# Kernel optimization log

Hardware: AMD Instinct MI355X
Metric: run time of the kernel (lower is better)

The kernel has to match this reference:

```python
import jax, jax.numpy as jnp
import numpy as np
from functools import partial

B, C, IMG, P = 16, 1, 512, 16
GRID = IMG // P           # 32
N = GRID * GRID           # 1024
E = 768
DEPTH = 12
H = 12
HD = E // H               # 64
FF = 4 * E                # 3072
NUM_KEEP = N // 2         # mask_ratio = 0.5
LN_EPS = 1e-5


def sincos_2d_pos_embed(embed_dim, grid_size):
    half = embed_dim // 2
    def emb1d(dim, pos):
        hd = dim // 2
        freq = jnp.exp(-np.log(10000.0) * jnp.arange(hd, dtype=jnp.float32) / hd)
        ang = pos[:, None] * freq[None, :]
        return jnp.concatenate([jnp.sin(ang), jnp.cos(ang)], axis=1)
    gh, gw = jnp.meshgrid(jnp.arange(grid_size, dtype=jnp.float32),
                          jnp.arange(grid_size, dtype=jnp.float32), indexing='ij')
    return jnp.concatenate([emb1d(half, gh.reshape(-1)), emb1d(half, gw.reshape(-1))], axis=1)


def setup_inputs() -> dict:
    key = jax.random.key(0)
    ks = jax.random.split(key, 16)
    std = 0.02
    d = {
        'x': jax.random.normal(ks[0], (B, C, IMG, IMG), jnp.float32),
        'noise': jax.random.uniform(ks[1], (B, N), jnp.float32),
        'patch_w': jax.random.normal(ks[2], (E, C, P, P), jnp.float32) * std,
        'patch_b': jnp.zeros((E,), jnp.float32),
        'pe_norm_w': jnp.ones((E,), jnp.float32),
        'pe_norm_b': jnp.zeros((E,), jnp.float32),
        'pos_embed': sincos_2d_pos_embed(E, GRID)[None],  # [1, N, E]
        'ln1_w': jnp.ones((DEPTH, E), jnp.float32),
        'ln1_b': jnp.zeros((DEPTH, E), jnp.float32),
        'qkv_w': jax.random.normal(ks[3], (DEPTH, 3 * E, E), jnp.float32) * std,
        'qkv_b': jnp.zeros((DEPTH, 3 * E), jnp.float32),
        'proj_w': jax.random.normal(ks[4], (DEPTH, E, E), jnp.float32) * std,
        'proj_b': jnp.zeros((DEPTH, E), jnp.float32),
        'ln2_w': jnp.ones((DEPTH, E), jnp.float32),
        'ln2_b': jnp.zeros((DEPTH, E), jnp.float32),
        'fc1_w': jax.random.normal(ks[5], (DEPTH, FF, E), jnp.float32) * std,
        'fc1_b': jnp.zeros((DEPTH, FF), jnp.float32),
        'fc2_w': jax.random.normal(ks[6], (DEPTH, E, FF), jnp.float32) * std,
        'fc2_b': jnp.zeros((DEPTH, E), jnp.float32),
        'norm_w': jnp.ones((E,), jnp.float32),
        'norm_b': jnp.zeros((E,), jnp.float32),
    }
    return d


def layernorm(x, w, b):
    m = jnp.mean(x, axis=-1, keepdims=True)
    v = jnp.mean(jnp.square(x - m), axis=-1, keepdims=True)
    return (x - m) * jax.lax.rsqrt(v + LN_EPS) * w + b


def transformer_block(x, p):
    ln1_w, ln1_b, qkv_w, qkv_b, proj_w, proj_b, ln2_w, ln2_b, fc1_w, fc1_b, fc2_w, fc2_b = p
    b, n, _ = x.shape
    h = layernorm(x, ln1_w, ln1_b)
    qkv = (h @ qkv_w.T + qkv_b).reshape(b, n, 3, H, HD)
    q, k, v = qkv[:, :, 0], qkv[:, :, 1], qkv[:, :, 2]          # [b, n, H, HD]
    scale = HD ** -0.5
    attn = jnp.einsum('bqhd,bkhd->bhqk', q, k) * scale
    attn = jax.nn.softmax(attn, axis=-1)
    o = jnp.einsum('bhqk,bkhd->bqhd', attn, v).reshape(b, n, E)
    x = x + (o @ proj_w.T + proj_b)
    h = layernorm(x, ln2_w, ln2_b)
    h = jax.nn.gelu(h @ fc1_w.T + fc1_b, approximate=False)
    x = x + (h @ fc2_w.T + fc2_b)
    return x


def reference(x, noise, patch_w, patch_b, pe_norm_w, pe_norm_b, pos_embed,
              ln1_w, ln1_b, qkv_w, qkv_b, proj_w, proj_b,
              ln2_w, ln2_b, fc1_w, fc1_b, fc2_w, fc2_b, norm_w, norm_b):
    b = x.shape[0]
    # Patch embedding: stride-P conv == patch extraction + matmul
    patches = x.reshape(b, C, GRID, P, GRID, P).transpose(0, 2, 4, 1, 3, 5)
    patches = patches.reshape(b, N, C * P * P)
    t = patches @ patch_w.reshape(E, -1).T + patch_b            # [b, N, E]
    t = layernorm(t, pe_norm_w, pe_norm_b)
    t = t + pos_embed
    # Random masking (mask_ratio = 0.5)
    ids_shuffle = jnp.argsort(noise, axis=1)
    ids_restore = jnp.argsort(ids_shuffle, axis=1)
    ids_keep = ids_shuffle[:, :NUM_KEEP]
    x_vis = jnp.take_along_axis(t, ids_keep[:, :, None], axis=1)  # [b, NUM_KEEP, E]
    mask = jnp.ones((b, N), jnp.float32).at[:, :NUM_KEEP].set(0.0)
    mask = jnp.take_along_axis(mask, ids_restore, axis=1)
    # Transformer blocks (scan over stacked per-layer params)
    stacked = (ln1_w, ln1_b, qkv_w, qkv_b, proj_w, proj_b,
               ln2_w, ln2_b, fc1_w, fc1_b, fc2_w, fc2_b)
    def body(carry, p):
        return transformer_block(carry, p), None
    x_vis, _ = jax.lax.scan(body, x_vis, stacked)
    x_vis = layernorm(x_vis, norm_w, norm_b)
    return x_vis, mask, ids_restore
```

## Files before the change

kernel.cpp:

```cpp
#include <hip/hip_runtime.h>
#include <hip/hip_bf16.h>
#include <cstddef>
#include <cstdint>

typedef unsigned short u16;
typedef __attribute__((ext_vector_type(8))) short short8;
typedef __attribute__((ext_vector_type(4))) float f32x4;

constexpr int BB   = 16;
constexpr int E    = 768;
constexpr int DEPTH= 12;
constexpr int NH   = 12;
constexpr int FF   = 3072;
constexpr int NTOK = 1024;
constexpr int KEEP = 512;
constexpr float LN_EPS = 1e-5f;

__device__ __forceinline__ u16 f2b(float f) {
    __hip_bfloat16 h = __float2bfloat16(f);
    return *reinterpret_cast<u16*>(&h);
}

__global__ __launch_bounds__(256)
void patchify16(const float* __restrict__ x, u16* __restrict__ patches) {
    int i = blockIdx.x * 256 + threadIdx.x;
    int k = i & 255;
    int n = (i >> 8) & 1023;
    int b = i >> 18;
    int gi = n >> 5, gj = n & 31;
    int pi = k >> 4, pj = k & 15;
    patches[i] = f2b(x[((size_t)b << 18) + (size_t)((gi << 4) + pi) * 512 + (gj << 4) + pj]);
}

__global__ __launch_bounds__(256)
void convert4(const float* __restrict__ s0, int n0, const float* __restrict__ s1, int n1,
              const float* __restrict__ s2, int n2, const float* __restrict__ s3, int n3,
              u16* __restrict__ dst, int total) {
    int i4 = (blockIdx.x * 256 + threadIdx.x) * 4;
    if (i4 >= total) return;
    const float* s; int off;
    if (i4 < n0) { s = s0; off = i4; }
    else if (i4 < n0 + n1) { s = s1; off = i4 - n0; }
    else if (i4 < n0 + n1 + n2) { s = s2; off = i4 - n0 - n1; }
    else { s = s3; off = i4 - n0 - n1 - n2; }
    float4 v = *(const float4*)(s + off);
    u16 u0 = f2b(v.x), u1 = f2b(v.y), u2 = f2b(v.z), u3 = f2b(v.w);
    u16 tmp[4] = {u0, u1, u2, u3};
    *(uint2*)(dst + i4) = *(uint2*)tmp;
}

__device__ __forceinline__ float block_sum256(float v, float* sh) {
    #pragma unroll
    for (int m = 32; m; m >>= 1) v += __shfl_xor(v, m, 64);
    int w = threadIdx.x >> 6;
    __syncthreads();
    if ((threadIdx.x & 63) == 0) sh[w] = v;
    __syncthreads();
    return sh[0] + sh[1] + sh[2] + sh[3];
}

template<bool OUTBF, bool POS>
__global__ __launch_bounds__(256)
void ln_kernel(const float* __restrict__ in, void* __restrict__ outp,
               const float* __restrict__ w, const float* __restrict__ bias,
               const float* __restrict__ pos) {
    __shared__ float sh[4];
    int tok = blockIdx.x, t = threadIdx.x;
    const float* row = in + (size_t)tok * E;
    float v0 = row[t], v1 = row[t + 256], v2 = row[t + 512];
    float s = block_sum256(v0 + v1 + v2, sh);
    float mean = s * (1.0f / 768.0f);
    float d0 = v0 - mean, d1 = v1 - mean, d2 = v2 - mean;
    float s2 = block_sum256(d0*d0 + d1*d1 + d2*d2, sh);
    float rstd = rsqrtf(s2 * (1.0f / 768.0f) + LN_EPS);
    float r0 = d0 * rstd * w[t]       + bias[t];
    float r1 = d1 * rstd * w[t + 256] + bias[t + 256];
    float r2 = d2 * rstd * w[t + 512] + bias[t + 512];
    if (POS) {
        int n = tok & (NTOK - 1);
        const float* prow = pos + (size_t)n * E;
        r0 += prow[t]; r1 += prow[t + 256]; r2 += prow[t + 512];
    }
    if (OUTBF) {
        u16* orow = (u16*)outp + (size_t)tok * E;
        orow[t] = f2b(r0); orow[t + 256] = f2b(r1); orow[t + 512] = f2b(r2);
    } else {
        float* orow = (float*)outp + (size_t)tok * E;
        orow[t] = r0; orow[t + 256] = r1; orow[t + 512] = r2;
    }
}

__global__ __launch_bounds__(1024)
void sort_kernel(const float* __restrict__ noise, int* __restrict__ ids_keep,
                 float* __restrict__ mask_out, float* __restrict__ restore_out) {
    __shared__ float sv[1024];
    __shared__ int   si[1024];
    int b = blockIdx.x, t = threadIdx.x;
    sv[t] = noise[b * 1024 + t];
    si[t] = t;
    __syncthreads();
    for (int k = 2; k <= 1024; k <<= 1) {
        for (int j = k >> 1; j > 0; j >>= 1) {
            int p = t ^ j;
            if (p > t) {
                bool up = ((t & k) == 0);
                float a = sv[t], c = sv[p];
                int ia = si[t], ic = si[p];
                bool sw = up ? (a > c || (a == c && ia > ic))
                             : (a < c || (a == c && ia < ic));
                if (sw) { sv[t] = c; sv[p] = a; si[t] = ic; si[p] = ia; }
            }
            __syncthreads();
        }
    }
    int idx = si[t];
    if (t < KEEP) ids_keep[b * KEEP + t] = idx;
    restore_out[b * 1024 + idx] = (float)t;
    mask_out[b * 1024 + idx] = (t < KEEP) ? 0.0f : 1.0f;
}

__global__ __launch_bounds__(256)
void gather_kernel(const float* __restrict__ t, const int* __restrict__ keep,
                   float* __restrict__ X) {
    int tok = blockIdx.x;
    int b = tok >> 9;
    int src = keep[tok];
    const float* s = t + ((size_t)(b << 10) + src) * E;
    float* d = X + (size_t)tok * E;
    int tid = threadIdx.x;
    d[tid]       = s[tid];
    d[tid + 256] = s[tid + 256];
    d[tid + 512] = s[tid + 512];
}

template<bool GELU, bool RES, bool OUTBF>
__global__ __launch_bounds__(256)
void mfma_gemm(const u16* __restrict__ A, const u16* __restrict__ W,
               const float* __restrict__ bias, const float* __restrict__ R,
               void* __restrict__ Cout, int M, int N, int K) {
    __shared__ u16 As[128 * 32];
    __shared__ u16 Ws[128 * 32];
    int tid = threadIdx.x;
    int lane = tid & 63, w = tid >> 6;
    int m0 = blockIdx.y << 7, n0 = blockIdx.x << 7;
    int wr = (w >> 1) << 6;
    int wc = (w & 1) << 6;
    int r16 = lane & 15, kq = lane >> 4;

    f32x4 acc[4][4];
    #pragma unroll
    for (int i = 0; i < 4; ++i)
        #pragma unroll
        for (int j = 0; j < 4; ++j) acc[i][j] = (f32x4)0.0f;

    int seg = w * 2;
    const u16* gA = A + (size_t)(m0 + seg * 16 + (lane >> 2)) * K + (lane & 3) * 8;
    const u16* gW = W + (size_t)(n0 + seg * 16 + (lane >> 2)) * K + (lane & 3) * 8;
    u16* lA = As + seg * 512;
    u16* lW = Ws + seg * 512;
    const size_t rowK16 = (size_t)16 * K;

    for (int k0 = 0; k0 < K; k0 += 32) {
        __syncthreads();
        __builtin_amdgcn_global_load_lds((const __attribute__((address_space(1))) void*)(gA + k0),
                                         (__attribute__((address_space(3))) void*)(lA), 16, 0, 0);
        __builtin_amdgcn_global_load_lds((const __attribute__((address_space(1))) void*)(gA + k0 + rowK16),
                                         (__attribute__((address_space(3))) void*)(lA + 512), 16, 0, 0);
        __builtin_amdgcn_global_load_lds((const __attribute__((address_space(1))) void*)(gW + k0),
                                         (__attribute__((address_space(3))) void*)(lW), 16, 0, 0);
        __builtin_amdgcn_global_load_lds((const __attribute__((address_space(1))) void*)(gW + k0 + rowK16),
                                         (__attribute__((address_space(3))) void*)(lW + 512), 16, 0, 0);
        __syncthreads();
        short8 af[4], bf[4];
        #pragma unroll
        for (int t = 0; t < 4; ++t) af[t] = *(const short8*)(As + (wr + t * 16 + r16) * 32 + kq * 8);
        #pragma unroll
        for (int t = 0; t < 4; ++t) bf[t] = *(const short8*)(Ws + (wc + t * 16 + r16) * 32 + kq * 8);
        #pragma unroll
        for (int i = 0; i < 4; ++i)
            #pragma unroll
            for (int j = 0; j < 4; ++j)
                acc[i][j] = __builtin_amdgcn_mfma_f32_16x16x32_bf16(af[i], bf[j], acc[i][j], 0, 0, 0);
    }

    #pragma unroll
    for (int i = 0; i < 4; ++i) {
        int row = m0 + wr + i * 16 + kq * 4;
        #pragma unroll
        for (int j = 0; j < 4; ++j) {
            int col = n0 + wc + j * 16 + r16;
            float bcol = bias[col];
            #pragma unroll
            for (int rg = 0; rg < 4; ++rg) {
                size_t off = (size_t)(row + rg) * N + col;
                float v = acc[i][j][rg] + bcol;
                if (GELU) v = 0.5f * v * (1.0f + erff(v * 0.70710678118654752f));
                if (RES)  v += R[off];
                if (OUTBF) ((u16*)Cout)[off] = f2b(v);
                else       ((float*)Cout)[off] = v;
            }
        }
    }
}

__global__ __launch_bounds__(256)
void attn_mfma(const u16* __restrict__ qkv, u16* __restrict__ out) {
    __shared__ u16 Ks[64 * 80];
    __shared__ u16 Vt[64 * 80];
    __shared__ u16 Ps[64 * 80];
    int tid = threadIdx.x, lane = tid & 63, w = tid >> 6;
    int bh = blockIdx.y;
    int b = bh / NH, h = bh - b * NH;
    int q0 = blockIdx.x << 6;
    int r16 = lane & 15, kq = lane >> 4;
    const u16* base = qkv + (size_t)b * 512 * 2304 + h * 64;

    const u16* qrow = base + (size_t)(q0 + w * 16 + r16) * 2304 + kq * 8;
    short8 qa0 = *(const short8*)(qrow);
    short8 qa1 = *(const short8*)(qrow + 32);

    f32x4 o[4];
    #pragma unroll
    for (int dt = 0; dt < 4; ++dt) o[dt] = (f32x4)0.0f;
    float mrow[4], lrow[4];
    #pragma unroll
    for (int r = 0; r < 4; ++r) { mrow[r] = -1e30f; lrow[r] = 0.0f; }

    for (int kt = 0; kt < 8; ++kt) {
        int k0 = kt << 6;
        __syncthreads();
        #pragma unroll
        for (int i = 0; i < 2; ++i) {
            int v = tid + 256 * i;
            int kp = v >> 3, d8 = (v & 7) * 8;
            short8 kv = *(const short8*)(base + (size_t)(k0 + kp) * 2304 + 768 + d8);
            *(short8*)(Ks + kp * 80 + d8) = kv;
            short8 vv = *(const short8*)(base + (size_t)(k0 + kp) * 2304 + 1536 + d8);
            #pragma unroll
            for (int j = 0; j < 8; ++j) Vt[(d8 + j) * 80 + kp] = (u16)vv[j];
        }
        __syncthreads();
        f32x4 s[4];
        #pragma unroll
        for (int ct = 0; ct < 4; ++ct) {
            short8 kb0 = *(const short8*)(Ks + (ct * 16 + r16) * 80 + kq * 8);
            short8 kb1 = *(const short8*)(Ks + (ct * 16 + r16) * 80 + kq * 8 + 32);
            s[ct] = (f32x4)0.0f;
            s[ct] = __builtin_amdgcn_mfma_f32_16x16x32_bf16(qa0, kb0, s[ct], 0, 0, 0);
            s[ct] = __builtin_amdgcn_mfma_f32_16x16x32_bf16(qa1, kb1, s[ct], 0, 0, 0);
            s[ct] *= 0.125f;
        }
        float alpha[4];
        #pragma unroll
        for (int r = 0; r < 4; ++r) {
            float mx = fmaxf(fmaxf(s[0][r], s[1][r]), fmaxf(s[2][r], s[3][r]));
            #pragma unroll
            for (int msk = 1; msk < 16; msk <<= 1) mx = fmaxf(mx, __shfl_xor(mx, msk, 64));
            float mnew = fmaxf(mrow[r], mx);
            alpha[r] = expf(mrow[r] - mnew);
            mrow[r] = mnew;
            float ls = 0.0f;
            #pragma unroll
            for (int ct = 0; ct < 4; ++ct) {
                float p = expf(s[ct][r] - mnew);
                s[ct][r] = p; ls += p;
            }
            #pragma unroll
            for (int msk = 1; msk < 16; msk <<= 1) ls += __shfl_xor(ls, msk, 64);
            lrow[r] = lrow[r] * alpha[r] + ls;
        }
        #pragma unroll
        for (int ct = 0; ct < 4; ++ct)
            #pragma unroll
            for (int r = 0; r < 4; ++r)
                Ps[(w * 16 + kq * 4 + r) * 80 + ct * 16 + r16] = f2b(s[ct][r]);
        #pragma unroll
        for (int dt = 0; dt < 4; ++dt)
            #pragma unroll
            for (int r = 0; r < 4; ++r) o[dt][r] *= alpha[r];
        short8 pa0 = *(const short8*)(Ps + (w * 16 + r16) * 80 + kq * 8);
        short8 pa1 = *(const short8*)(Ps + (w * 16 + r16) * 80 + kq * 8 + 32);
        #pragma unroll
        for (int dt = 0; dt < 4; ++dt) {
            short8 vb0 = *(const short8*)(Vt + (dt * 16 + r16) * 80 + kq * 8);
            short8 vb1 = *(const short8*)(Vt + (dt * 16 + r16) * 80 + kq * 8 + 32);
            o[dt] = __builtin_amdgcn_mfma_f32_16x16x32_bf16(pa0, vb0, o[dt], 0, 0, 0);
            o[dt] = __builtin_amdgcn_mfma_f32_16x16x32_bf16(pa1, vb1, o[dt], 0, 0, 0);
        }
    }
    #pragma unroll
    for (int dt = 0; dt < 4; ++dt)
        #pragma unroll
        for (int r = 0; r < 4; ++r) {
            float val = o[dt][r] / lrow[r];
            int row = q0 + w * 16 + kq * 4 + r;
            out[((size_t)b * 512 + row) * 768 + h * 64 + dt * 16 + r16] = f2b(val);
        }
}

extern "C" void kernel_launch(void* const* d_in, const int* in_sizes, int n_in,
                              void* d_out, int out_size, void* d_ws, size_t ws_size,
                              hipStream_t stream) {
    const float* x       = (const float*)d_in[0];
    const float* noise   = (const float*)d_in[1];
    const float* patch_w = (const float*)d_in[2];
    const float* patch_b = (const float*)d_in[3];
    const float* pe_w    = (const float*)d_in[4];
    const float* pe_b    = (const float*)d_in[5];
    const float* pos     = (const float*)d_in[6];
    const float* ln1_w   = (const float*)d_in[7];
    const float* ln1_b   = (const float*)d_in[8];
    const float* qkv_w   = (const float*)d_in[9];
    const float* qkv_b   = (const float*)d_in[10];
    const float* proj_w  = (const float*)d_in[11];
    const float* proj_b  = (const float*)d_in[12];
    const float* ln2_w   = (const float*)d_in[13];
    const float* ln2_b   = (const float*)d_in[14];
    const float* fc1_w   = (const float*)d_in[15];
    const float* fc1_b   = (const float*)d_in[16];
    const float* fc2_w   = (const float*)d_in[17];
    const float* fc2_b   = (const float*)d_in[18];
    const float* norm_w  = (const float*)d_in[19];
    const float* norm_b  = (const float*)d_in[20];

    float* out = (float*)d_out;
    char* ws = (char*)d_ws;

    float* X     = (float*)(ws + 0);
    u16*   Hb16  = (u16*)  (ws + 25165824);
    u16*   QKV16 = (u16*)  (ws + 37748736);
    u16*   FF16  = (u16*)  (ws + 75497472);
    u16*   AO16  = (u16*)  (ws + 125829120);
    u16*   wbuf  = (u16*)  (ws + 138412032);
    u16*   pwbuf = (u16*)  (ws + 152567808);
    int*   keep  = (int*)  (ws + 152961024);
    float* tfull   = (float*)QKV16;
    u16*   pat16   = (u16*)(ws + 88080384);

    float* mask_out    = out + (size_t)BB * KEEP * E;
    float* restore_out = mask_out + BB * NTOK;

    const int n_qkv = 3 * E * E;
    const int n_prj = E * E;
    const int n_fc  = FF * E;
    u16* wq  = wbuf;
    u16* wp  = wbuf + n_qkv;
    u16* wf1 = wbuf + n_qkv + n_prj;
    u16* wf2 = wbuf + n_qkv + n_prj + n_fc;
    const int wtot = n_qkv + n_prj + 2 * n_fc;

    convert4<<<192, 256, 0, stream>>>(patch_w, E * 256, patch_w, 0, patch_w, 0, patch_w, 0,
                                      pwbuf, E * 256);
    patchify16<<<16384, 256, 0, stream>>>(x, pat16);
    mfma_gemm<false, false, false><<<dim3(E / 128, (BB * NTOK) / 128), 256, 0, stream>>>(
        pat16, pwbuf, patch_b, nullptr, tfull, BB * NTOK, E, 256);
    ln_kernel<false, true><<<BB * NTOK, 256, 0, stream>>>(tfull, tfull, pe_w, pe_b, pos);
    sort_kernel<<<BB, 1024, 0, stream>>>(noise, keep, mask_out, restore_out);
    gather_kernel<<<BB * KEEP, 256, 0, stream>>>(tfull, keep, X);

    const int M = BB * KEEP;
    for (int l = 0; l < DEPTH; ++l) {
        convert4<<<wtot / 1024, 256, 0, stream>>>(
            qkv_w + (size_t)l * n_qkv, n_qkv, proj_w + (size_t)l * n_prj, n_prj,
            fc1_w + (size_t)l * n_fc, n_fc,  fc2_w + (size_t)l * n_fc, n_fc,
            wbuf, wtot);
        ln_kernel<true, false><<<M, 256, 0, stream>>>(X, Hb16, ln1_w + l * E, ln1_b + l * E, nullptr);
        mfma_gemm<false, false, true><<<dim3((3 * E) / 128, M / 128), 256, 0, stream>>>(
            Hb16, wq, qkv_b + (size_t)l * 3 * E, nullptr, QKV16, M, 3 * E, E);
        attn_mfma<<<dim3(KEEP / 64, BB * NH), 256, 0, stream>>>(QKV16, AO16);
        mfma_gemm<false, true, false><<<dim3(E / 128, M / 128), 256, 0, stream>>>(
            AO16, wp, proj_b + (size_t)l * E, X, X, M, E, E);
        ln_kernel<true, false><<<M, 256, 0, stream>>>(X, Hb16, ln2_w + l * E, ln2_b + l * E, nullptr);
        mfma_gemm<true, false, true><<<dim3(FF / 128, M / 128), 256, 0, stream>>>(
            Hb16, wf1, fc1_b + (size_t)l * FF, nullptr, FF16, M, FF, E);
        mfma_gemm<false, true, false><<<dim3(E / 128, M / 128), 256, 0, stream>>>(
            FF16, wf2, fc2_b + (size_t)l * E, X, X, M, E, FF);
    }
    ln_kernel<false, false><<<M, 256, 0, stream>>>(X, out, norm_w, norm_b, nullptr);
}
```

Baseline: 4.227 ms.

## Replace GEMM with 256x256-tile 8-wave double-buffered pipelined MFMA kernel

Replaces the 128x128 single-buffered MFMA GEMM with a 256x256-tile kernel using 8 waves, 128KB of LDS double buffering, XOR-swizzled LDS layout, and staged global_load_lds prefetch interleaved with MFMA phases via raw barriers and setprio. It also remaps block IDs with an XCD-aware swizzle. The intent is to overlap global loads with compute, raise data reuse per tile, and avoid LDS bank conflicts. Larger tiles reduce the block count for the small N=768 GEMMs (e.g. 96 blocks for proj/fc2), which risks leaving CUs idle.

```diff
diff --git a/kernel.cpp b/kernel.cpp
--- a/kernel.cpp
+++ b/kernel.cpp
@@ -20,6 +20,8 @@
     __hip_bfloat16 h = __float2bfloat16(f);
     return *reinterpret_cast<u16*>(&h);
 }
+
+#define BARRIER() asm volatile("s_barrier" ::: "memory")
 
 __global__ __launch_bounds__(256)
 void patchify16(const float* __restrict__ x, u16* __restrict__ patches) {
@@ -44,8 +46,7 @@
     else if (i4 < n0 + n1 + n2) { s = s2; off = i4 - n0 - n1; }
     else { s = s3; off = i4 - n0 - n1 - n2; }
     float4 v = *(const float4*)(s + off);
-    u16 u0 = f2b(v.x), u1 = f2b(v.y), u2 = f2b(v.z), u3 = f2b(v.w);
-    u16 tmp[4] = {u0, u1, u2, u3};
+    u16 tmp[4] = {f2b(v.x), f2b(v.y), f2b(v.z), f2b(v.w)};
     *(uint2*)(dst + i4) = *(uint2*)tmp;
 }
 
@@ -134,66 +135,130 @@
 }
 
 template<bool GELU, bool RES, bool OUTBF>
-__global__ __launch_bounds__(256)
-void mfma_gemm(const u16* __restrict__ A, const u16* __restrict__ W,
-               const float* __restrict__ bias, const float* __restrict__ R,
-               void* __restrict__ Cout, int M, int N, int K) {
-    __shared__ u16 As[128 * 32];
-    __shared__ u16 Ws[128 * 32];
-    int tid = threadIdx.x;
-    int lane = tid & 63, w = tid >> 6;
-    int m0 = blockIdx.y << 7, n0 = blockIdx.x << 7;
-    int wr = (w >> 1) << 6;
-    int wc = (w & 1) << 6;
-    int r16 = lane & 15, kq = lane >> 4;
-
-    f32x4 acc[4][4];
-    #pragma unroll
-    for (int i = 0; i < 4; ++i)
+__global__ __launch_bounds__(512, 2)
+void gemm8(const u16* __restrict__ A, const u16* __restrict__ W,
+           const float* __restrict__ bias, const float* __restrict__ R,
+           void* __restrict__ Cout, int M, int N, int K) {
+    __shared__ u16 lds[65536];
+    const int tid = threadIdx.x;
+    const int l = tid & 63, w = tid >> 6;
+    const int wm = w >> 2, wn = w & 3;
+    const int r16 = l & 15, kq = l >> 4;
+    const int rc   = (kq ^ ((r16 >> 1) & 3)) * 8;
+    const int cswz = ((l & 3) ^ ((l >> 3) & 3)) * 8;
+
+    const int nbc = N >> 8;
+    const int nwg = gridDim.x;
+    const int bid = blockIdx.x;
+    const int swz = (bid & 7) * (nwg >> 3) + (bid >> 3);
+    const int m0 = (swz / nbc) << 8, n0 = (swz % nbc) << 8;
+
+    const int rA = m0 + w * 16 + (l >> 2);
+    const int rB = n0 + w * 16 + (l >> 2);
+    const u16* a0 = A + (size_t)rA * K + cswz;
+    const u16* a1 = A + (size_t)(rA + 128) * K + cswz;
+    const u16* b0 = W + (size_t)rB * K + cswz;
+    const u16* b1 = W + (size_t)(rB + 128) * K + cswz;
+    const int dstw = w * 512;
+
+    auto stage = [&](int part, int koff, const u16* s0, const u16* s1) {
+        u16* d = &lds[part * 8192 + dstw];
+        __builtin_amdgcn_global_load_lds((const __attribute__((address_space(1))) void*)(s0 + koff),
+                                         (__attribute__((address_space(3))) void*)d, 16, 0, 0);
+        __builtin_amdgcn_global_load_lds((const __attribute__((address_space(1))) void*)(s1 + koff),
+                                         (__attribute__((address_space(3))) void*)(d + 4096), 16, 0, 0);
+    };
+
+    f32x4 acc[8][4];
+    #pragma unroll
+    for (int i = 0; i < 8; ++i)
         #pragma unroll
         for (int j = 0; j < 4; ++j) acc[i][j] = (f32x4)0.0f;
 
-    int seg = w * 2;
-    const u16* gA = A + (size_t)(m0 + seg * 16 + (lane >> 2)) * K + (lane & 3) * 8;
-    const u16* gW = W + (size_t)(n0 + seg * 16 + (lane >> 2)) * K + (lane & 3) * 8;
-    u16* lA = As + seg * 512;
-    u16* lW = Ws + seg * 512;
-    const size_t rowK16 = (size_t)16 * K;
-
-    for (int k0 = 0; k0 < K; k0 += 32) {
-        __syncthreads();
-        __builtin_amdgcn_global_load_lds((const __attribute__((address_space(1))) void*)(gA + k0),
-                                         (__attribute__((address_space(3))) void*)(lA), 16, 0, 0);
-        __builtin_amdgcn_global_load_lds((const __attribute__((address_space(1))) void*)(gA + k0 + rowK16),
-                                         (__attribute__((address_space(3))) void*)(lA + 512), 16, 0, 0);
-        __builtin_amdgcn_global_load_lds((const __attribute__((address_space(1))) void*)(gW + k0),
-                                         (__attribute__((address_space(3))) void*)(lW), 16, 0, 0);
-        __builtin_amdgcn_global_load_lds((const __attribute__((address_space(1))) void*)(gW + k0 + rowK16),
-                                         (__attribute__((address_space(3))) void*)(lW + 512), 16, 0, 0);
-        __syncthreads();
-        short8 af[4], bf[4];
-        #pragma unroll
-        for (int t = 0; t < 4; ++t) af[t] = *(const short8*)(As + (wr + t * 16 + r16) * 32 + kq * 8);
-        #pragma unroll
-        for (int t = 0; t < 4; ++t) bf[t] = *(const short8*)(Ws + (wc + t * 16 + r16) * 32 + kq * 8);
-        #pragma unroll
-        for (int i = 0; i < 4; ++i)
-            #pragma unroll
-            for (int j = 0; j < 4; ++j)
-                acc[i][j] = __builtin_amdgcn_mfma_f32_16x16x32_bf16(af[i], bf[j], acc[i][j], 0, 0, 0);
-    }
-
-    #pragma unroll
-    for (int i = 0; i < 4; ++i) {
-        int row = m0 + wr + i * 16 + kq * 4;
-        #pragma unroll
-        for (int j = 0; j < 4; ++j) {
-            int col = n0 + wc + j * 16 + r16;
-            float bcol = bias[col];
+    short8 af[4], bf[4];
+    auto rdA = [&](int reg, int mh) {
+        const u16* p = &lds[reg * 8192 + (wm * 128 + mh * 64 + r16) * 32 + rc];
+        af[0] = *(const short8*)(p);
+        af[1] = *(const short8*)(p + 512);
+        af[2] = *(const short8*)(p + 1024);
+        af[3] = *(const short8*)(p + 1536);
+    };
+    auto rdB = [&](int reg) {
+        const u16* p = &lds[reg * 8192 + (wn * 64 + r16) * 32 + rc];
+        bf[0] = *(const short8*)(p);
+        bf[1] = *(const short8*)(p + 512);
+        bf[2] = *(const short8*)(p + 1024);
+        bf[3] = *(const short8*)(p + 1536);
+    };
+    auto mma16 = [&](int fo) {
+        #pragma unroll
+        for (int f = 0; f < 4; ++f)
+            #pragma unroll
+            for (int g = 0; g < 4; ++g)
+                acc[fo + f][g] = __builtin_amdgcn_mfma_f32_16x16x32_bf16(af[f], bf[g], acc[fo + f][g], 0, 0, 0);
+    };
+
+    const int NK = K >> 6;
+    stage(0, 0,  a0, a1);
+    stage(2, 0,  b0, b1);
+    stage(1, 32, a0, a1);
+    stage(3, 32, b0, b1);
+    asm volatile("s_waitcnt vmcnt(4)" ::: "memory");
+    BARRIER();
+
+    for (int kt = 0; kt < NK; ++kt) {
+        const int curb = (kt & 1) * 4, nxtb = curb ^ 4;
+        const bool hn = (kt + 1) < NK;
+        const int kn = (kt + 1) << 6;
+        rdA(curb + 0, 0);
+        rdB(curb + 2);
+        if (hn) stage(nxtb + 0, kn, a0, a1);
+        BARRIER();
+        __builtin_amdgcn_s_setprio(1);
+        mma16(0);
+        __builtin_amdgcn_s_setprio(0);
+        BARRIER();
+        rdA(curb + 0, 1);
+        if (hn) stage(nxtb + 2, kn, b0, b1);
+        BARRIER();
+        __builtin_amdgcn_s_setprio(1);
+        mma16(4);
+        __builtin_amdgcn_s_setprio(0);
+        if (hn) asm volatile("s_waitcnt vmcnt(4)" ::: "memory");
+        else    asm volatile("s_waitcnt vmcnt(0)" ::: "memory");
+        BARRIER();
+        rdA(curb + 1, 0);
+        rdB(curb + 3);
+        if (hn) stage(nxtb + 1, kn + 32, a0, a1);
+        BARRIER();
+        __builtin_amdgcn_s_setprio(1);
+        mma16(0);
+        __builtin_amdgcn_s_setprio(0);
+        BARRIER();
+        rdA(curb + 1, 1);
+        if (hn) stage(nxtb + 3, kn + 32, b0, b1);
+        BARRIER();
+        __builtin_amdgcn_s_setprio(1);
+        mma16(4);
+        __builtin_amdgcn_s_setprio(0);
+        if (hn) asm volatile("s_waitcnt vmcnt(4)" ::: "memory");
+        else    asm volatile("s_waitcnt vmcnt(0)" ::: "memory");
+        BARRIER();
+    }
+
+    float bcol[4];
+    #pragma unroll
+    for (int g = 0; g < 4; ++g) bcol[g] = bias[n0 + wn * 64 + g * 16 + r16];
+    #pragma unroll
+    for (int f = 0; f < 8; ++f) {
+        int row = m0 + wm * 128 + f * 16 + kq * 4;
+        #pragma unroll
+        for (int g = 0; g < 4; ++g) {
+            int col = n0 + wn * 64 + g * 16 + r16;
             #pragma unroll
             for (int rg = 0; rg < 4; ++rg) {
                 size_t off = (size_t)(row + rg) * N + col;
-                float v = acc[i][j][rg] + bcol;
+                float v = acc[f][g][rg] + bcol[g];
                 if (GELU) v = 0.5f * v * (1.0f + erff(v * 0.70710678118654752f));
                 if (RES)  v += R[off];
                 if (OUTBF) ((u16*)Cout)[off] = f2b(v);
@@ -352,7 +417,7 @@
     convert4<<<192, 256, 0, stream>>>(patch_w, E * 256, patch_w, 0, patch_w, 0, patch_w, 0,
                                       pwbuf, E * 256);
     patchify16<<<16384, 256, 0, stream>>>(x, pat16);
-    mfma_gemm<false, false, false><<<dim3(E / 128, (BB * NTOK) / 128), 256, 0, stream>>>(
+    gemm8<false, false, false><<<(16384/256)*(768/256), 512, 0, stream>>>(
         pat16, pwbuf, patch_b, nullptr, tfull, BB * NTOK, E, 256);
     ln_kernel<false, true><<<BB * NTOK, 256, 0, stream>>>(tfull, tfull, pe_w, pe_b, pos);
     sort_kernel<<<BB, 1024, 0, stream>>>(noise, keep, mask_out, restore_out);
@@ -365,15 +430,15 @@
             fc1_w + (size_t)l * n_fc, n_fc,  fc2_w + (size_t)l * n_fc, n_fc,
             wbuf, wtot);
         ln_kernel<true, false><<<M, 256, 0, stream>>>(X, Hb16, ln1_w + l * E, ln1_b + l * E, nullptr);
-        mfma_gemm<false, false, true><<<dim3((3 * E) / 128, M / 128), 256, 0, stream>>>(
+        gemm8<false, false, true><<<(M/256)*((3*E)/256), 512, 0, stream>>>(
             Hb16, wq, qkv_b + (size_t)l * 3 * E, nullptr, QKV16, M, 3 * E, E);
         attn_mfma<<<dim3(KEEP / 64, BB * NH), 256, 0, stream>>>(QKV16, AO16);
-        mfma_gemm<false, true, false><<<dim3(E / 128, M / 128), 256, 0, stream>>>(
+        gemm8<false, true, false><<<(M/256)*(E/256), 512, 0, stream>>>(
             AO16, wp, proj_b + (size_t)l * E, X, X, M, E, E);
         ln_kernel<true, false><<<M, 256, 0, stream>>>(X, Hb16, ln2_w + l * E, ln2_b + l * E, nullptr);
-        mfma_gemm<true, false, true><<<dim3(FF / 128, M / 128), 256, 0, stream>>>(
+        gemm8<true, false, true><<<(M/256)*(FF/256), 512, 0, stream>>>(
             Hb16, wf1, fc1_b + (size_t)l * FF, nullptr, FF16, M, FF, E);
-        mfma_gemm<false, true, false><<<dim3(E / 128, M / 128), 256, 0, stream>>>(
+        gemm8<false, true, false><<<(M/256)*(E/256), 512, 0, stream>>>(
             FF16, wf2, fc2_b + (size_t)l * E, X, X, M, E, FF);
     }
     ln_kernel<false, false><<<M, 256, 0, stream>>>(X, out, norm_w, norm_b, nullptr);
```

New measurement: 4.544 ms. +7.5%, slower.
